# Kernel tuning notes

Hardware: AMD Instinct MI355X
Metric: run time of the kernel (lower is better)

Reference implementation:

```python
import jax, jax.numpy as jnp
import numpy as np

B, N, D = 16, 512, 512
H, DH = 8, 64
INNER = H * DH            # attention inner dim = 512
FF = 4 * D                # feedforward hidden = 2048
CI = 2 * D                # conv expansion inner = 1024
K = 31                    # depthwise kernel
MAXPOS = 512
EPS = 1e-5                # LayerNorm / BatchNorm eps (torch defaults)
PAD = (K // 2, K // 2 - (K + 1) % 2)  # calc_same_padding(31) -> (15, 15)


def _ln(x, g, b):
    m = x.mean(-1, keepdims=True)
    v = ((x - m) ** 2).mean(-1, keepdims=True)
    return (x - m) / jnp.sqrt(v + EPS) * g + b


def _swish(x):
    return x * jax.nn.sigmoid(x)


def setup_inputs() -> dict:
    key = jax.random.key(0)
    ks = jax.random.split(key, 16)
    s = 0.02
    inp = {
        'x': jax.random.normal(ks[0], (B, N, D), jnp.float32),
        # FF1
        'ff1_ln_g': jnp.ones((D,), jnp.float32), 'ff1_ln_b': jnp.zeros((D,), jnp.float32),
        'ff1_w1': jax.random.normal(ks[1], (D, FF), jnp.float32) * s,
        'ff1_b1': jnp.zeros((FF,), jnp.float32),
        'ff1_w2': jax.random.normal(ks[2], (FF, D), jnp.float32) * s,
        'ff1_b2': jnp.zeros((D,), jnp.float32),
        # Attention
        'attn_ln_g': jnp.ones((D,), jnp.float32), 'attn_ln_b': jnp.zeros((D,), jnp.float32),
        'qkv_w': jax.random.normal(ks[3], (D, 3 * INNER), jnp.float32) * s,
        'out_w': jax.random.normal(ks[4], (INNER, D), jnp.float32) * s,
        'rel_emb': jax.random.normal(ks[5], (2 * MAXPOS + 1, DH), jnp.float32) * s,
        # Conv module
        'conv_ln_g': jnp.ones((D,), jnp.float32), 'conv_ln_b': jnp.zeros((D,), jnp.float32),
        'pw1_w': jax.random.normal(ks[6], (2 * CI, D), jnp.float32) * s,
        'pw1_b': jnp.zeros((2 * CI,), jnp.float32),
        'dw_w': jax.random.normal(ks[7], (CI, 1, K), jnp.float32) * s,
        'dw_b': jnp.zeros((CI,), jnp.float32),
        'bn_g': jnp.ones((CI,), jnp.float32), 'bn_b': jnp.zeros((CI,), jnp.float32),
        'bn_mean': jnp.zeros((CI,), jnp.float32), 'bn_var': jnp.ones((CI,), jnp.float32),
        'pw2_w': jax.random.normal(ks[8], (D, CI), jnp.float32) * s,
        'pw2_b': jnp.zeros((D,), jnp.float32),
        # FF2
        'ff2_ln_g': jnp.ones((D,), jnp.float32), 'ff2_ln_b': jnp.zeros((D,), jnp.float32),
        'ff2_w1': jax.random.normal(ks[9], (D, FF), jnp.float32) * s,
        'ff2_b1': jnp.zeros((FF,), jnp.float32),
        'ff2_w2': jax.random.normal(ks[10], (FF, D), jnp.float32) * s,
        'ff2_b2': jnp.zeros((D,), jnp.float32),
        # post norm
        'post_ln_g': jnp.ones((D,), jnp.float32), 'post_ln_b': jnp.zeros((D,), jnp.float32),
    }
    return inp


def _ff(x, g, b, w1, b1, w2, b2):
    h = _ln(x, g, b)
    h = _swish(h @ w1 + b1)
    return h @ w2 + b2


def _attention(x, g, b, qkv_w, out_w, rel_emb):
    n = x.shape[1]
    scale = DH ** (-0.5)
    h = _ln(x, g, b)
    qkv = h @ qkv_w                                    # [b,n,3*inner]
    q, k, v = jnp.split(qkv, 3, axis=-1)
    q = q.reshape(B, n, H, DH).transpose(0, 2, 1, 3)   # [b,h,n,d]
    k = k.reshape(B, n, H, DH).transpose(0, 2, 1, 3)
    v = v.reshape(B, n, H, DH).transpose(0, 2, 1, 3)
    dots = jnp.einsum('bhnd,bhmd->bhnm', q, k) * scale
    seq = jnp.arange(n)
    dist = jnp.clip(seq[:, None] - seq[None, :], -MAXPOS, MAXPOS) + MAXPOS  # [n,n]
    rpe = rel_emb[dist]                                # [n,r,d]
    pos = jnp.einsum('bhnd,nrd->bhnr', q, rpe) * scale
    sim = dots + pos
    attn = jax.nn.softmax(sim.astype(jnp.float32), axis=-1).astype(q.dtype)
    out = jnp.einsum('bhnm,bhmd->bhnd', attn, v)
    out = out.transpose(0, 2, 1, 3).reshape(B, n, INNER)
    return out @ out_w


def _conv_module(x, ln_g, ln_b, pw1_w, pw1_b, dw_w, dw_b, bn_g, bn_b, bn_mean, bn_var, pw2_w, pw2_b):
    h = _ln(x, ln_g, ln_b)                             # [b,n,c]
    h = h.transpose(0, 2, 1)                           # [b,c,n]
    h = jnp.einsum('oc,bcn->bon', pw1_w, h) + pw1_b[:, None]  # pointwise conv1 -> [b,2ci,n]
    out, gate = jnp.split(h, 2, axis=1)
    h = out * jax.nn.sigmoid(gate)                     # GLU -> [b,ci,n]
    h = jnp.pad(h, ((0, 0), (0, 0), PAD))
    h = jax.lax.conv_general_dilated(
        h, dw_w, window_strides=(1,), padding='VALID',
        feature_group_count=CI, dimension_numbers=('NCH', 'OIH', 'NCH'))
    h = h + dw_b[:, None]
    # BatchNorm1d eval-mode with running stats
    h = (h - bn_mean[:, None]) / jnp.sqrt(bn_var[:, None] + EPS) * bn_g[:, None] + bn_b[:, None]
    h = _swish(h)
    h = jnp.einsum('oc,bcn->bon', pw2_w, h) + pw2_b[:, None]  # pointwise conv2 -> [b,d,n]
    return h.transpose(0, 2, 1)


def reference(x, ff1_ln_g, ff1_ln_b, ff1_w1, ff1_b1, ff1_w2, ff1_b2,
              attn_ln_g, attn_ln_b, qkv_w, out_w, rel_emb,
              conv_ln_g, conv_ln_b, pw1_w, pw1_b, dw_w, dw_b,
              bn_g, bn_b, bn_mean, bn_var, pw2_w, pw2_b,
              ff2_ln_g, ff2_ln_b, ff2_w1, ff2_b1, ff2_w2, ff2_b2,
              post_ln_g, post_ln_b):
    x = 0.5 * _ff(x, ff1_ln_g, ff1_ln_b, ff1_w1, ff1_b1, ff1_w2, ff1_b2) + x
    x = _attention(x, attn_ln_g, attn_ln_b, qkv_w, out_w, rel_emb) + x
    x = _conv_module(x, conv_ln_g, conv_ln_b, pw1_w, pw1_b, dw_w, dw_b,
                     bn_g, bn_b, bn_mean, bn_var, pw2_w, pw2_b) + x
    x = 0.5 * _ff(x, ff2_ln_g, ff2_ln_b, ff2_w1, ff2_b1, ff2_w2, ff2_b2) + x
    return _ln(x, post_ln_g, post_ln_b)
```

## Files before the change

### kernel.cpp

```cpp
#include <hip/hip_runtime.h>
#include <stdint.h>

#define ROWS 8192
#define N_ 512

typedef __attribute__((ext_vector_type(4))) float f32x4;
typedef __attribute__((ext_vector_type(8))) short s16x8;
typedef __attribute__((ext_vector_type(4))) short s16x4;
typedef __attribute__((ext_vector_type(4))) unsigned short u16x4;
typedef __attribute__((ext_vector_type(8))) unsigned short u16x8;

__device__ __forceinline__ float bf2f(unsigned short h){
  union { unsigned int u; float f; } v; v.u = ((unsigned int)h) << 16; return v.f;
}
__device__ __forceinline__ unsigned short f2bf(float f){
  union { float f; unsigned int u; } v; v.f = f;
  unsigned int r = v.u + 0x7FFFu + ((v.u >> 16) & 1u);
  return (unsigned short)(r >> 16);
}
__device__ __forceinline__ float sigm(float x){ return 1.f / (1.f + __expf(-x)); }
__device__ __forceinline__ unsigned cvtpk(float lo, float hi){
  unsigned r;
  asm("v_cvt_pk_bf16_f32 %0, %1, %2" : "=v"(r) : "v"(lo), "v"(hi));
  return r;
}
__device__ __forceinline__ void gload16(const void* g, void* l){
  __builtin_amdgcn_global_load_lds(
    (const __attribute__((address_space(1))) void*)g,
    (__attribute__((address_space(3))) void*)l, 16, 0, 0);
}

__global__ void k_transpose_cvt(const float* __restrict__ in, unsigned short* __restrict__ out,
                                int R, int C){
  __shared__ float t[32][33];
  int c0 = blockIdx.x*32, r0 = blockIdx.y*32;
  int tx = threadIdx.x & 31, ty = threadIdx.x >> 5;
  #pragma unroll
  for(int i=0;i<32;i+=8) t[ty+i][tx] = in[(size_t)(r0+ty+i)*C + c0+tx];
  __syncthreads();
  #pragma unroll
  for(int i=0;i<32;i+=8) out[(size_t)(c0+ty+i)*R + r0+tx] = f2bf(t[tx][ty+i]);
}

__global__ void k_cvt(const float* __restrict__ in, unsigned short* __restrict__ out, int n){
  int i = blockIdx.x*256 + threadIdx.x;
  if(i < n) out[i] = f2bf(in[i]);
}

template<int OUTF32>
__global__ void k_ln(const float* __restrict__ x, const float* __restrict__ gw,
                     const float* __restrict__ bw, void* __restrict__ outp){
  const int row = blockIdx.x*4 + (threadIdx.x >> 6);
  const int lane = threadIdx.x & 63;
  const f32x4* xr = (const f32x4*)(x + (size_t)row*512);
  f32x4 v0 = xr[lane], v1 = xr[lane + 64];
  float s  = v0[0]+v0[1]+v0[2]+v0[3] + v1[0]+v1[1]+v1[2]+v1[3];
  float s2 = v0[0]*v0[0]+v0[1]*v0[1]+v0[2]*v0[2]+v0[3]*v0[3]
           + v1[0]*v1[0]+v1[1]*v1[1]+v1[2]*v1[2]+v1[3]*v1[3];
  #pragma unroll
  for(int off=1; off<64; off<<=1){ s += __shfl_xor(s, off); s2 += __shfl_xor(s2, off); }
  float mean = s * (1.f/512.f);
  float inv = rsqrtf(s2*(1.f/512.f) - mean*mean + 1e-5f);
  const f32x4* gv = (const f32x4*)gw; const f32x4* bv = (const f32x4*)bw;
  f32x4 g0 = gv[lane], g1 = gv[lane+64], b0 = bv[lane], b1 = bv[lane+64];
  f32x4 o0, o1;
  #pragma unroll
  for(int e=0;e<4;e++){ o0[e] = (v0[e]-mean)*inv*g0[e] + b0[e];
                        o1[e] = (v1[e]-mean)*inv*g1[e] + b1[e]; }
  if(OUTF32){
    f32x4* op = (f32x4*)((float*)outp + (size_t)row*512);
    op[lane] = o0; op[lane+64] = o1;
  } else {
    unsigned short* ob = (unsigned short*)outp + (size_t)row*512;
    s16x4 h0, h1;
    #pragma unroll
    for(int e=0;e<4;e++){ h0[e] = (short)f2bf(o0[e]); h1[e] = (short)f2bf(o1[e]); }
    *(s16x4*)(ob + lane*4) = h0;
    *(s16x4*)(ob + 256 + lane*4) = h1;
  }
}

template<int EPI>
__global__ __launch_bounds__(256, 2)
void k_gemm(const unsigned short* __restrict__ A, const unsigned short* __restrict__ Bt,
            const float* __restrict__ bias, const float* __restrict__ res,
            void* __restrict__ outp, unsigned short* __restrict__ vt, int M, int N, int K){
  __shared__ alignas(16) unsigned short As[128*64];
  __shared__ alignas(16) unsigned short Bs[128*64];
  const int tid = threadIdx.x, lane = tid & 63, wave = tid >> 6;
  const int nwg = gridDim.x * gridDim.y;
  int orig = blockIdx.x + gridDim.x * blockIdx.y;
  int q8 = nwg >> 3, r8 = nwg & 7, xcd = orig & 7, idx = orig >> 3;
  int wg = (xcd < r8 ? xcd * (q8 + 1) : r8 * (q8 + 1) + (xcd - r8) * q8) + idx;
  const int m0 = (wg / gridDim.x) * 128, n0 = (wg % gridDim.x) * 128;
  const int wm = (wave >> 1) * 64, wn = (wave & 1) * 64;
  f32x4 acc[4][4];
  #pragma unroll
  for(int a=0;a<4;a++)
    #pragma unroll
    for(int b=0;b<4;b++) acc[a][b] = (f32x4){0.f,0.f,0.f,0.f};

  for(int kt = 0; kt < K; kt += 64){
    #pragma unroll
    for(int i=0;i<4;i++){
      int flat = i*256 + tid;
      int r = flat >> 3;
      int cs = ((flat & 7) ^ (r & 7)) << 3;
      gload16(A  + (size_t)(m0 + r)*K + kt + cs, &As[flat*8]);
      gload16(Bt + (size_t)(n0 + r)*K + kt + cs, &Bs[flat*8]);
    }
    __syncthreads();
    #pragma unroll
    for(int ks=0; ks<2; ks++){
      s16x8 af[4], bfr[4];
      #pragma unroll
      for(int mi=0;mi<4;mi++){
        int row = wm + mi*16 + (lane & 15);
        int ch = (ks*4 + (lane >> 4)) ^ (row & 7);
        af[mi] = *(const s16x8*)(&As[row*64 + ch*8]);
      }
      #pragma unroll
      for(int ni=0;ni<4;ni++){
        int row = wn + ni*16 + (lane & 15);
        int ch = (ks*4 + (lane >> 4)) ^ (row & 7);
        bfr[ni] = *(const s16x8*)(&Bs[row*64 + ch*8]);
      }
      #pragma unroll
      for(int mi=0;mi<4;mi++)
        #pragma unroll
        for(int ni=0;ni<4;ni++)
          acc[mi][ni] = __builtin_amdgcn_mfma_f32_16x16x32_bf16(af[mi], bfr[ni], acc[mi][ni], 0, 0, 0);
    }
    __syncthreads();
  }
  const int rb = (lane >> 4) * 4, cb = lane & 15;
  #pragma unroll
  for(int mi=0;mi<4;mi++){
    #pragma unroll
    for(int ni=0;ni<4;ni++){
      int col = n0 + wn + ni*16 + cb;
      int rowbase = m0 + wm + mi*16 + rb;
      if(EPI==6 && col >= 1024){
        u16x4 tv;
        #pragma unroll
        for(int r=0;r<4;r++) tv[r] = f2bf(acc[mi][ni][r]);
        int bb = rowbase >> 9, n = rowbase & 511;
        *(u16x4*)(vt + (((size_t)(bb*512 + col - 1024)) << 9) + n) = tv;
      } else {
        #pragma unroll
        for(int r=0;r<4;r++){
          int row = rowbase + r;
          float v = acc[mi][ni][r];
          if(EPI==1||EPI==2||EPI==4||EPI==5) v += bias[col];
          if(EPI==2) v = 0.5f*v + res[(size_t)row*N + col];
          if(EPI==3||EPI==5) v += res[(size_t)row*N + col];
          if(EPI==1) v = v * sigm(v);
          if(EPI==0||EPI==1||EPI==4||EPI==6) ((unsigned short*)outp)[(size_t)row*N + col] = f2bf(v);
          else                               ((float*)outp)[(size_t)row*N + col] = v;
        }
      }
    }
  }
}

__global__ __launch_bounds__(512, 2)
void k_attn(const unsigned short* __restrict__ qkv, const unsigned short* __restrict__ vt,
            const unsigned short* __restrict__ emb, unsigned short* __restrict__ outb){
  __shared__ alignas(16) unsigned short Ks[512*64];
  const int tid = threadIdx.x, lane = tid & 63, w = tid >> 6;
  const int q0 = blockIdx.x * 128, h = blockIdx.y, b = blockIdx.z;
  const int j = lane & 15, g = lane >> 4;
  const int n0w = q0 + w*16;
  const size_t qkvbase = (size_t)b*N_*1536;

  #pragma unroll
  for(int i=0;i<8;i++){
    int flat = i*512 + tid;
    int r = flat >> 3;
    int cs = ((flat & 7) ^ (r & 7)) << 3;
    gload16(qkv + qkvbase + (size_t)r*1536 + 512 + h*64 + cs, &Ks[flat*8]);
  }
  s16x8 qf[2];
  #pragma unroll
  for(int ks=0;ks<2;ks++)
    qf[ks] = *(const s16x8*)(qkv + qkvbase + (size_t)(n0w + j)*1536 + h*64 + ks*32 + g*8);
  __syncthreads();

  const float C2 = 0.125f * 1.4426950408889634f;

  f32x4 pa1 = {0.f,0.f,0.f,0.f};
  #pragma unroll
  for(int ks=0;ks<2;ks++){
    s16x8 e1 = *(const s16x8*)(emb + (size_t)(n0w + 513 + j)*64 + ks*32 + g*8);
    pa1 = __builtin_amdgcn_mfma_f32_16x16x32_bf16(e1, qf[ks], pa1, 0,0,0);
  }
  float mx = -1e30f;
  #pragma unroll
  for(int rt=0;rt<32;rt++){
    const int cb = n0w - rt*16 + 512;
    f32x4 s   = {0.f,0.f,0.f,0.f};
    f32x4 pa0 = {0.f,0.f,0.f,0.f};
    #pragma unroll
    for(int ks=0;ks<2;ks++){
      int row = rt*16 + j;
      int ch = (ks*4 + g) ^ (row & 7);
      s16x8 kf = *(const s16x8*)(&Ks[row*64 + (ch<<3)]);
      s = __builtin_amdgcn_mfma_f32_16x16x32_bf16(kf, qf[ks], s, 0,0,0);
      s16x8 e0 = *(const s16x8*)(emb + (size_t)(cb - 15 + j)*64 + ks*32 + g*8);
      pa0 = __builtin_amdgcn_mfma_f32_16x16x32_bf16(e0, qf[ks], pa0, 0,0,0);
    }
    #pragma unroll
    for(int reg=0;reg<4;reg++){
      int elem = (j + 3 - reg) & 3;
      float s0 = (elem & 2) ? ((elem & 1) ? pa0[3] : pa0[2]) : ((elem & 1) ? pa0[1] : pa0[0]);
      float s1 = (elem & 2) ? ((elem & 1) ? pa1[3] : pa1[2]) : ((elem & 1) ? pa1[1] : pa1[0]);
      int m = j + 15 - g*4 - reg;
      int src = j + (((m & 15) >> 2) << 4);
      float v0 = __shfl(s0, src);
      float v1 = __shfl(s1, src);
      mx = fmaxf(mx, s[reg] + (m < 16 ? v0 : v1));
    }
    pa1 = pa0;
  }
  mx = fmaxf(mx, __shfl_xor(mx, 16));
  mx = fmaxf(mx, __shfl_xor(mx, 32));
  const float mc = mx * C2;

  pa1 = (f32x4){0.f,0.f,0.f,0.f};
  #pragma unroll
  for(int ks=0;ks<2;ks++){
    s16x8 e1 = *(const s16x8*)(emb + (size_t)(n0w + 513 + j)*64 + ks*32 + g*8);
    pa1 = __builtin_amdgcn_mfma_f32_16x16x32_bf16(e1, qf[ks], pa1, 0,0,0);
  }
  float l = 0.f;
  f32x4 o[4];
  #pragma unroll
  for(int dt=0;dt<4;dt++) o[dt] = (f32x4){0.f,0.f,0.f,0.f};
  const unsigned short* vbase = vt + (((size_t)(b*8 + h)) << 15);
  const int srcA = j + ((g & 1) << 5);
  const int srcB = srcA + 16;
  const bool hi = (g >= 2);

  #pragma unroll
  for(int rts=0; rts<16; rts++){
    unsigned wp[4];
    #pragma unroll
    for(int sub=0; sub<2; sub++){
      const int rt = rts*2 + sub;
      const int cb = n0w - rt*16 + 512;
      f32x4 s   = {0.f,0.f,0.f,0.f};
      f32x4 pa0 = {0.f,0.f,0.f,0.f};
      #pragma unroll
      for(int ks=0;ks<2;ks++){
        int row = rt*16 + j;
        int ch = (ks*4 + g) ^ (row & 7);
        s16x8 kf = *(const s16x8*)(&Ks[row*64 + (ch<<3)]);
        s = __builtin_amdgcn_mfma_f32_16x16x32_bf16(kf, qf[ks], s, 0,0,0);
        s16x8 e0 = *(const s16x8*)(emb + (size_t)(cb - 15 + j)*64 + ks*32 + g*8);
        pa0 = __builtin_amdgcn_mfma_f32_16x16x32_bf16(e0, qf[ks], pa0, 0,0,0);
      }
      f32x4 sc;
      #pragma unroll
      for(int reg=0;reg<4;reg++){
        int elem = (j + 3 - reg) & 3;
        float s0 = (elem & 2) ? ((elem & 1) ? pa0[3] : pa0[2]) : ((elem & 1) ? pa0[1] : pa0[0]);
        float s1 = (elem & 2) ? ((elem & 1) ? pa1[3] : pa1[2]) : ((elem & 1) ? pa1[1] : pa1[0]);
        int m = j + 15 - g*4 - reg;
        int src = j + (((m & 15) >> 2) << 4);
        float v0 = __shfl(s0, src);
        float v1 = __shfl(s1, src);
        sc[reg] = s[reg] + (m < 16 ? v0 : v1);
      }
      pa1 = pa0;
      float p0 = exp2f(fmaf(sc[0], C2, -mc));
      float p1 = exp2f(fmaf(sc[1], C2, -mc));
      float p2 = exp2f(fmaf(sc[2], C2, -mc));
      float p3 = exp2f(fmaf(sc[3], C2, -mc));
      l += (p0 + p1) + (p2 + p3);
      wp[sub*2]   = cvtpk(p0, p1);
      wp[sub*2+1] = cvtpk(p2, p3);
    }
    unsigned a0 = __shfl(wp[0], srcA);
    unsigned a1 = __shfl(wp[1], srcA);
    unsigned a2 = __shfl(wp[0], srcB);
    unsigned a3 = __shfl(wp[1], srcB);
    unsigned b0 = __shfl(wp[2], srcA);
    unsigned b1 = __shfl(wp[3], srcA);
    unsigned b2 = __shfl(wp[2], srcB);
    unsigned b3 = __shfl(wp[3], srcB);
    union { unsigned u[4]; s16x8 v; } pu;
    pu.u[0] = hi ? b0 : a0;
    pu.u[1] = hi ? b1 : a1;
    pu.u[2] = hi ? b2 : a2;
    pu.u[3] = hi ? b3 : a3;
    #pragma unroll
    for(int dt=0;dt<4;dt++){
      int d = dt*16 + j;
      s16x8 vf = *(const s16x8*)(vbase + (size_t)d*512 + rts*32 + g*8);
      o[dt] = __builtin_amdgcn_mfma_f32_16x16x32_bf16(pu.v, vf, o[dt], 0,0,0);
    }
  }
  l += __shfl_xor(l, 16);
  l += __shfl_xor(l, 32);
  float inv = 1.f / l;
  #pragma unroll
  for(int reg=0;reg<4;reg++){
    float invq = __shfl(inv, (g<<2) + reg);
    int tok = n0w + (g<<2) + reg;
    #pragma unroll
    for(int dt=0;dt<4;dt++)
      outb[(size_t)(b*N_ + tok)*512 + h*64 + dt*16 + j] = f2bf(o[dt][reg] * invq);
  }
}

__global__ void k_glu(const unsigned short* __restrict__ hid, unsigned short* __restrict__ outp){
  size_t i = (size_t)blockIdx.x*256 + threadIdx.x;
  int row = (int)(i >> 7), cc = (int)(i & 127);
  u16x8 a  = *(const u16x8*)(hid + (size_t)row*2048 + cc*8);
  u16x8 gt = *(const u16x8*)(hid + (size_t)row*2048 + 1024 + cc*8);
  u16x8 o;
  #pragma unroll
  for(int e=0;e<8;e++){
    float av = bf2f(a[e]), gv = bf2f(gt[e]);
    o[e] = f2bf(av * sigm(gv));
  }
  *(u16x8*)(outp + (size_t)row*1024 + cc*8) = o;
}

__global__ __launch_bounds__(256, 2)
void k_dwconv(const unsigned short* __restrict__ gin, const float* __restrict__ dww,
              const float* __restrict__ dwb, const float* __restrict__ bng,
              const float* __restrict__ bnb, const float* __restrict__ bnm,
              const float* __restrict__ bnv, unsigned short* __restrict__ outp){
  __shared__ unsigned short gl[94][136];
  __shared__ float wl[31][128];
  const int c0 = blockIdx.x*128, n0 = blockIdx.y*64, b = blockIdx.z;
  const int tid = threadIdx.x;
  for(int i=0;i<6;i++){
    int flat = i*256 + tid;
    if(flat < 94*16){
      int r = flat >> 4, c = flat & 15;
      int n = n0 - 15 + r;
      u16x8 v = {0,0,0,0,0,0,0,0};
      if(n >= 0 && n < 512) v = *(const u16x8*)(gin + (size_t)(b*512 + n)*1024 + c0 + c*8);
      *(u16x8*)(&gl[r][c*8]) = v;
    }
  }
  for(int i=0;i<16;i++){
    int flat = i*256 + tid;
    if(flat < 31*128){
      int t = flat >> 7, cc = flat & 127;
      wl[t][cc] = dww[(size_t)(c0 + cc)*31 + t];
    }
  }
  __syncthreads();
  const int tc = tid & 31, tn = tid >> 5;
  f32x4 acc[8];
  #pragma unroll
  for(int nn=0;nn<8;nn++) acc[nn] = (f32x4){0.f,0.f,0.f,0.f};
  for(int t=0;t<31;t++){
    f32x4 wv = *(const f32x4*)(&wl[t][tc*4]);
    #pragma unroll
    for(int nn=0;nn<8;nn++){
      s16x4 gv = *(const s16x4*)(&gl[tn*8 + nn + t][tc*4]);
      f32x4 g4 = { bf2f((unsigned short)gv[0]), bf2f((unsigned short)gv[1]),
                   bf2f((unsigned short)gv[2]), bf2f((unsigned short)gv[3]) };
      acc[nn] += g4 * wv;
    }
  }
  #pragma unroll
  for(int e=0;e<4;e++){
    int c = c0 + tc*4 + e;
    float s  = bng[c] * rsqrtf(bnv[c] + 1e-5f);
    float sh = bnb[c] - bnm[c]*s;
    float db = dwb[c];
    #pragma unroll
    for(int nn=0;nn<8;nn++){
      float v = (acc[nn][e] + db)*s + sh;
      v = v * sigm(v);
      outp[(size_t)(b*512 + n0 + tn*8 + nn)*1024 + c] = f2bf(v);
    }
  }
}

extern "C" void kernel_launch(void* const* d_in, const int* in_sizes, int n_in,
                              void* d_out, int out_size, void* d_ws, size_t ws_size,
                              hipStream_t stream){
  const float* x        = (const float*)d_in[0];
  const float* ff1_ln_g = (const float*)d_in[1];
  const float* ff1_ln_b = (const float*)d_in[2];
  const float* ff1_w1   = (const float*)d_in[3];
  const float* ff1_b1   = (const float*)d_in[4];
  const float* ff1_w2   = (const float*)d_in[5];
  const float* ff1_b2   = (const float*)d_in[6];
  const float* attn_ln_g= (const float*)d_in[7];
  const float* attn_ln_b= (const float*)d_in[8];
  const float* qkv_w    = (const float*)d_in[9];
  const float* out_w    = (const float*)d_in[10];
  const float* rel_emb  = (const float*)d_in[11];
  const float* conv_ln_g= (const float*)d_in[12];
  const float* conv_ln_b= (const float*)d_in[13];
  const float* pw1_w    = (const float*)d_in[14];
  const float* pw1_b    = (const float*)d_in[15];
  const float* dw_w     = (const float*)d_in[16];
  const float* dw_b     = (const float*)d_in[17];
  const float* bn_g     = (const float*)d_in[18];
  const float* bn_b     = (const float*)d_in[19];
  const float* bn_mean  = (const float*)d_in[20];
  const float* bn_var   = (const float*)d_in[21];
  const float* pw2_w    = (const float*)d_in[22];
  const float* pw2_b    = (const float*)d_in[23];
  const float* ff2_ln_g = (const float*)d_in[24];
  const float* ff2_ln_b = (const float*)d_in[25];
  const float* ff2_w1   = (const float*)d_in[26];
  const float* ff2_b1   = (const float*)d_in[27];
  const float* ff2_w2   = (const float*)d_in[28];
  const float* ff2_b2   = (const float*)d_in[29];
  const float* post_ln_g= (const float*)d_in[30];
  const float* post_ln_b= (const float*)d_in[31];
  (void)in_sizes; (void)n_in; (void)out_size; (void)ws_size;

  char* ws = (char*)d_ws;
  size_t off = 0;
  auto alloc = [&](size_t bytes)->char*{ char* p = ws + off; off += (bytes + 255) & ~(size_t)255; return p; };
  float*          res  = (float*)         alloc((size_t)ROWS*512*4);
  unsigned short* hbuf = (unsigned short*)alloc((size_t)ROWS*512*2);
  unsigned short* hid  = (unsigned short*)alloc((size_t)ROWS*2048*2);
  unsigned short* qkvb = (unsigned short*)alloc((size_t)ROWS*1536*2);
  unsigned short* glub = (unsigned short*)alloc((size_t)ROWS*1024*2);
  unsigned short* attnout = glub;
  unsigned short* dwout   = qkvb;
  unsigned short* vtb     = hid;
  unsigned short* w1t  = (unsigned short*)alloc((size_t)2048*512*2);
  unsigned short* w2t  = (unsigned short*)alloc((size_t)2048*512*2);
  unsigned short* qkvt = (unsigned short*)alloc((size_t)1536*512*2);
  unsigned short* outt = (unsigned short*)alloc((size_t)512*512*2);
  unsigned short* pw1c = (unsigned short*)alloc((size_t)2048*512*2);
  unsigned short* pw2c = (unsigned short*)alloc((size_t)512*1024*2);
  unsigned short* f2w1t= (unsigned short*)alloc((size_t)2048*512*2);
  unsigned short* f2w2t= (unsigned short*)alloc((size_t)2048*512*2);
  unsigned short* rele = (unsigned short*)alloc((size_t)1025*64*2);

  k_transpose_cvt<<<dim3(64, 16), 256, 0, stream>>>(ff1_w1, w1t, 512, 2048);
  k_transpose_cvt<<<dim3(16, 64), 256, 0, stream>>>(ff1_w2, w2t, 2048, 512);
  k_transpose_cvt<<<dim3(48, 16), 256, 0, stream>>>(qkv_w, qkvt, 512, 1536);
  k_transpose_cvt<<<dim3(16, 16), 256, 0, stream>>>(out_w, outt, 512, 512);
  k_transpose_cvt<<<dim3(64, 16), 256, 0, stream>>>(ff2_w1, f2w1t, 512, 2048);
  k_transpose_cvt<<<dim3(16, 64), 256, 0, stream>>>(ff2_w2, f2w2t, 2048, 512);
  k_cvt<<<2048*512/256, 256, 0, stream>>>(pw1_w, pw1c, 2048*512);
  k_cvt<<<512*1024/256, 256, 0, stream>>>(pw2_w, pw2c, 512*1024);
  k_cvt<<<(1025*64+255)/256, 256, 0, stream>>>(rel_emb, rele, 1025*64);

  k_ln<0><<<ROWS/4, 256, 0, stream>>>(x, ff1_ln_g, ff1_ln_b, hbuf);
  k_gemm<1><<<dim3(16, 64), 256, 0, stream>>>(hbuf, w1t, ff1_b1, nullptr, hid, nullptr, ROWS, 2048, 512);
  k_gemm<2><<<dim3(4, 64), 256, 0, stream>>>(hid, w2t, ff1_b2, x, res, nullptr, ROWS, 512, 2048);
  k_ln<0><<<ROWS/4, 256, 0, stream>>>(res, attn_ln_g, attn_ln_b, hbuf);
  k_gemm<6><<<dim3(12, 64), 256, 0, stream>>>(hbuf, qkvt, nullptr, nullptr, qkvb, vtb, ROWS, 1536, 512);
  k_attn<<<dim3(4, 8, 16), 512, 0, stream>>>(qkvb, vtb, rele, attnout);
  k_gemm<3><<<dim3(4, 64), 256, 0, stream>>>(attnout, outt, nullptr, res, res, nullptr, ROWS, 512, 512);
  k_ln<0><<<ROWS/4, 256, 0, stream>>>(res, conv_ln_g, conv_ln_b, hbuf);
  k_gemm<4><<<dim3(16, 64), 256, 0, stream>>>(hbuf, pw1c, pw1_b, nullptr, hid, nullptr, ROWS, 2048, 512);
  k_glu<<<ROWS*128/256, 256, 0, stream>>>(hid, glub);
  k_dwconv<<<dim3(8, 8, 16), 256, 0, stream>>>(glub, dw_w, dw_b, bn_g, bn_b, bn_mean, bn_var, dwout);
  k_gemm<5><<<dim3(4, 64), 256, 0, stream>>>(dwout, pw2c, pw2_b, res, res, nullptr, ROWS, 512, 1024);
  k_ln<0><<<ROWS/4, 256, 0, stream>>>(res, ff2_ln_g, ff2_ln_b, hbuf);
  k_gemm<1><<<dim3(16, 64), 256, 0, stream>>>(hbuf, f2w1t, ff2_b1, nullptr, hid, nullptr, ROWS, 2048, 512);
  k_gemm<2><<<dim3(4, 64), 256, 0, stream>>>(hid, f2w2t, ff2_b2, res, res, nullptr, ROWS, 512, 2048);
  k_ln<1><<<ROWS/4, 256, 0, stream>>>(res, post_ln_g, post_ln_b, d_out);
}
```

Baseline: 496.3 us.

## Replace two-pass softmax with online softmax using lazy rescaling

```diff
diff --git a/kernel.cpp b/kernel.cpp
--- a/kernel.cpp
+++ b/kernel.cpp
@@ -194,45 +194,8 @@
     s16x8 e1 = *(const s16x8*)(emb + (size_t)(n0w + 513 + j)*64 + ks*32 + g*8);
     pa1 = __builtin_amdgcn_mfma_f32_16x16x32_bf16(e1, qf[ks], pa1, 0,0,0);
   }
-  float mx = -1e30f;
-  #pragma unroll
-  for(int rt=0;rt<32;rt++){
-    const int cb = n0w - rt*16 + 512;
-    f32x4 s   = {0.f,0.f,0.f,0.f};
-    f32x4 pa0 = {0.f,0.f,0.f,0.f};
-    #pragma unroll
-    for(int ks=0;ks<2;ks++){
-      int row = rt*16 + j;
-      int ch = (ks*4 + g) ^ (row & 7);
-      s16x8 kf = *(const s16x8*)(&Ks[row*64 + (ch<<3)]);
-      s = __builtin_amdgcn_mfma_f32_16x16x32_bf16(kf, qf[ks], s, 0,0,0);
-      s16x8 e0 = *(const s16x8*)(emb + (size_t)(cb - 15 + j)*64 + ks*32 + g*8);
-      pa0 = __builtin_amdgcn_mfma_f32_16x16x32_bf16(e0, qf[ks], pa0, 0,0,0);
-    }
-    #pragma unroll
-    for(int reg=0;reg<4;reg++){
-      int elem = (j + 3 - reg) & 3;
-      float s0 = (elem & 2) ? ((elem & 1) ? pa0[3] : pa0[2]) : ((elem & 1) ? pa0[1] : pa0[0]);
-      float s1 = (elem & 2) ? ((elem & 1) ? pa1[3] : pa1[2]) : ((elem & 1) ? pa1[1] : pa1[0]);
-      int m = j + 15 - g*4 - reg;
-      int src = j + (((m & 15) >> 2) << 4);
-      float v0 = __shfl(s0, src);
-      float v1 = __shfl(s1, src);
-      mx = fmaxf(mx, s[reg] + (m < 16 ? v0 : v1));
-    }
-    pa1 = pa0;
-  }
-  mx = fmaxf(mx, __shfl_xor(mx, 16));
-  mx = fmaxf(mx, __shfl_xor(mx, 32));
-  const float mc = mx * C2;
-
-  pa1 = (f32x4){0.f,0.f,0.f,0.f};
-  #pragma unroll
-  for(int ks=0;ks<2;ks++){
-    s16x8 e1 = *(const s16x8*)(emb + (size_t)(n0w + 513 + j)*64 + ks*32 + g*8);
-    pa1 = __builtin_amdgcn_mfma_f32_16x16x32_bf16(e1, qf[ks], pa1, 0,0,0);
-  }
-  float l = 0.f;
+
+  float m = -1e30f, l = 0.f;
   f32x4 o[4];
   #pragma unroll
   for(int dt=0;dt<4;dt++) o[dt] = (f32x4){0.f,0.f,0.f,0.f};
@@ -243,7 +206,7 @@
 
   #pragma unroll
   for(int rts=0; rts<16; rts++){
-    unsigned wp[4];
+    f32x4 scs[2];
     #pragma unroll
     for(int sub=0; sub<2; sub++){
       const int rt = rts*2 + sub;
@@ -259,23 +222,43 @@
         s16x8 e0 = *(const s16x8*)(emb + (size_t)(cb - 15 + j)*64 + ks*32 + g*8);
         pa0 = __builtin_amdgcn_mfma_f32_16x16x32_bf16(e0, qf[ks], pa0, 0,0,0);
       }
-      f32x4 sc;
       #pragma unroll
       for(int reg=0;reg<4;reg++){
         int elem = (j + 3 - reg) & 3;
         float s0 = (elem & 2) ? ((elem & 1) ? pa0[3] : pa0[2]) : ((elem & 1) ? pa0[1] : pa0[0]);
         float s1 = (elem & 2) ? ((elem & 1) ? pa1[3] : pa1[2]) : ((elem & 1) ? pa1[1] : pa1[0]);
-        int m = j + 15 - g*4 - reg;
-        int src = j + (((m & 15) >> 2) << 4);
+        int mm = j + 15 - g*4 - reg;
+        int src = j + (((mm & 15) >> 2) << 4);
         float v0 = __shfl(s0, src);
         float v1 = __shfl(s1, src);
-        sc[reg] = s[reg] + (m < 16 ? v0 : v1);
+        scs[sub][reg] = s[reg] + (mm < 16 ? v0 : v1);
       }
       pa1 = pa0;
-      float p0 = exp2f(fmaf(sc[0], C2, -mc));
-      float p1 = exp2f(fmaf(sc[1], C2, -mc));
-      float p2 = exp2f(fmaf(sc[2], C2, -mc));
-      float p3 = exp2f(fmaf(sc[3], C2, -mc));
+    }
+    float tmax = fmaxf(fmaxf(fmaxf(scs[0][0], scs[0][1]), fmaxf(scs[0][2], scs[0][3])),
+                       fmaxf(fmaxf(scs[1][0], scs[1][1]), fmaxf(scs[1][2], scs[1][3])));
+    tmax = fmaxf(tmax, __shfl_xor(tmax, 16));
+    tmax = fmaxf(tmax, __shfl_xor(tmax, 32));
+    if(__any(tmax > m + 48.f)){
+      float mn = fmaxf(m, tmax);
+      float f = exp2f((m - mn)*C2);
+      l *= f;
+      #pragma unroll
+      for(int reg=0;reg<4;reg++){
+        float fr = __shfl(f, (g<<2) + reg);
+        #pragma unroll
+        for(int dt=0;dt<4;dt++) o[dt][reg] *= fr;
+      }
+      m = mn;
+    }
+    const float mc = m * C2;
+    unsigned wp[4];
+    #pragma unroll
+    for(int sub=0; sub<2; sub++){
+      float p0 = exp2f(fmaf(scs[sub][0], C2, -mc));
+      float p1 = exp2f(fmaf(scs[sub][1], C2, -mc));
+      float p2 = exp2f(fmaf(scs[sub][2], C2, -mc));
+      float p3 = exp2f(fmaf(scs[sub][3], C2, -mc));
       l += (p0 + p1) + (p2 + p3);
       wp[sub*2]   = cvtpk(p0, p1);
       wp[sub*2+1] = cvtpk(p2, p3);
```

After: 482.4 us. 1.03x faster.
